# Performance work log

Hardware: AMD Instinct MI355X
Metric: run time of the kernel (lower is better)

Reference implementation:

```python
import jax, jax.numpy as jnp
import numpy as np

B, C, N_OUT = 8, 64, 65536
N_IN = 262144  # unpooled (input) spatial size
K, P = 9, 4    # kernel_size, bilinear interp points


def setup_inputs() -> dict:
    key = jax.random.key(0)
    k1, k2, k3, k4 = jax.random.split(key, 4)
    x = jax.random.normal(k1, (B, C, N_OUT), dtype=jnp.float32)
    idx_mask = jax.random.randint(k2, (B, C, N_OUT), 0, K, dtype=jnp.int32)
    sample_map = jax.random.randint(k3, (N_OUT, K, P), 0, N_IN, dtype=jnp.int32)
    interp_weights = jax.random.uniform(k4, (N_OUT, K, P), dtype=jnp.float32)
    return {"x": x, "idx_mask": idx_mask, "sample_map": sample_map,
            "interp_weights": interp_weights}


def reference(x, idx_mask, sample_map, interp_weights):
    # x: [B,C,N_out] pooled values; idx_mask: [B,C,N_out] winning kernel tap
    # sample_map: [N_out,K,P] int indices into flattened unpooled domain
    # interp_weights: [N_out,K,P] interpolation weights
    b, c, n_out = x.shape
    o_idx = jnp.arange(n_out)[None, None, :]               # [1,1,N_out]
    sel_map = sample_map[o_idx, idx_mask]                  # [B,C,N_out,P]
    sel_w = interp_weights[o_idx, idx_mask]                # [B,C,N_out,P]
    contrib = sel_w * x[..., None]                         # [B,C,N_out,P]
    out = jnp.zeros((b, c, N_IN), dtype=x.dtype)
    bi = jnp.arange(b)[:, None, None, None]
    ci = jnp.arange(c)[None, :, None, None]
    out = out.at[bi, ci, sel_map].add(contrib)             # scatter-add unpool
    return out
```

## Files before the change

kernel.cpp:

```cpp
#include <hip/hip_runtime.h>

#define BB      8
#define CC      64
#define N_OUT   65536
#define N_IN    262144
#define KK      9
#define PP      4
#define NE      (N_OUT * KK * PP)
#define NPLANES 512
#define CHUNK   16
#define NCHUNKS (N_IN / CHUNK)
#define NKEY    NCHUNKS
#define GTH     512
#define NS      (GTH / 32)
#define NFB     128
#define EPB     (NE / NFB)
#define XSTRIDE 800

typedef float f4_t __attribute__((ext_vector_type(4)));

#define WS_OFFSETS 0
#define WS_TOT     16400
#define WS_PRIV    32784
#define WS_HDR     (32784 + NFB * NKEY)
#define WS_ENTR    (2129936 + N_OUT * KK)
#define WS_XK      (((2719760 + 2 * NE) + 31) & ~31)
#define WS_END     (WS_XK + N_OUT * XSTRIDE)

#define XKTILE 16
#define XPAD   520
__global__ __launch_bounds__(256) void k_xk(const float* __restrict__ x,
                                            const int*   __restrict__ idx,
                                            unsigned* __restrict__ xk,
                                            unsigned* __restrict__ hdr) {
    __shared__ float xs[XKTILE * XPAD];
    __shared__ unsigned char ks[XKTILE * XPAD];
    __shared__ unsigned ot[XKTILE * 512];
    __shared__ int cnt[XKTILE][12];
    __shared__ int cur[XKTILE][12];
    __shared__ int cstart[XKTILE][12];
    __shared__ int pstart[XKTILE][12];
    const int t = threadIdx.x;
    const int obase = blockIdx.x * XKTILE;

    for (int i = t; i < XKTILE * 12; i += 256) cnt[i / 12][i % 12] = 0;

    for (int i = t; i < 512 * (XKTILE / 4); i += 256) {
        int p = i >> 2, q = i & 3;
        const size_t g = (size_t)p * N_OUT + obase + 4 * q;
        float4 xv = *(const float4*)(x + g);
        int4   kv = *(const int4*)(idx + g);
        int b = (4 * q) * XPAD + p;
        xs[b] = xv.x; xs[b + XPAD] = xv.y; xs[b + 2 * XPAD] = xv.z; xs[b + 3 * XPAD] = xv.w;
        ks[b] = (unsigned char)kv.x; ks[b + XPAD] = (unsigned char)kv.y;
        ks[b + 2 * XPAD] = (unsigned char)kv.z; ks[b + 3 * XPAD] = (unsigned char)kv.w;
    }
    __syncthreads();
    for (int i = t; i < XKTILE * 512; i += 256) {
        int oo = i >> 9, p = i & 511;
        atomicAdd(&cnt[oo][ks[oo * XPAD + p]], 1);
    }
    __syncthreads();
    if (t < XKTILE) {
        int s = 0, sp = 0;
        for (int k = 0; k < KK; ++k) {
            int c = cnt[t][k];
            cstart[t][k] = s;
            cur[t][k] = s;
            pstart[t][k] = sp;
            hdr[(size_t)(obase + t) * KK + k] = (unsigned)(sp | (c << 16));
            s += c;
            sp += (c + 31) & ~31;
        }
        cstart[t][KK] = 512;
    }
    __syncthreads();
    for (int i = t; i < XKTILE * 512; i += 256) {
        int oo = i >> 9, p = i & 511;
        int k = ks[oo * XPAD + p];
        int pos = atomicAdd(&cur[oo][k], 1);
        unsigned xb = __float_as_uint(xs[oo * XPAD + p]);
        ot[(oo << 9) + pos] = (xb & 0xFFFFFE00u) | (unsigned)p;
    }
    __syncthreads();
    for (int i = t; i < XKTILE * 512; i += 256) {
        int oo = i >> 9, pos = i & 511;
        int k = 0;
        while (k < KK - 1 && pos >= cstart[oo][k + 1]) ++k;
        int dst = pstart[oo][k] + (pos - cstart[oo][k]);
        xk[(size_t)(obase + oo) * XSTRIDE + dst] = ot[(oo << 9) + pos];
    }
}

__global__ __launch_bounds__(1024) void k_histA(const int* __restrict__ smap,
                                                int* __restrict__ priv) {
    __shared__ int h[NKEY];
    const int b = blockIdx.x;
    const int t = threadIdx.x;
    for (int i = t; i < NKEY; i += 1024) h[i] = 0;
    __syncthreads();
    const int e0 = b * EPB;
    #pragma unroll 2
    for (int i = 0; i < EPB / 1024; ++i)
        atomicAdd(&h[smap[e0 + i * 1024 + t] >> 4], 1);
    __syncthreads();
    for (int i = t; i < NKEY; i += 1024) priv[b * NKEY + i] = h[i];
}

__global__ __launch_bounds__(1024) void k_colscan(int* __restrict__ priv,
                                                  int* __restrict__ tot) {
    const int key = blockIdx.x * 1024 + threadIdx.x;
    int run = 0;
    for (int b = 0; b < NFB; ++b) {
        int* p = priv + b * NKEY + key;
        int v = *p; *p = run; run += v;
    }
    tot[key] = run;
}

__global__ __launch_bounds__(1024) void k_scan16k(const int* __restrict__ tot,
                                                  int* __restrict__ offsets) {
    __shared__ int sw[1024];
    const int t = threadIdx.x;
    int4 q0 = ((const int4*)tot)[4 * t + 0];
    int4 q1 = ((const int4*)tot)[4 * t + 1];
    int4 q2 = ((const int4*)tot)[4 * t + 2];
    int4 q3 = ((const int4*)tot)[4 * t + 3];
    int vals[16] = {q0.x, q0.y, q0.z, q0.w, q1.x, q1.y, q1.z, q1.w,
                    q2.x, q2.y, q2.z, q2.w, q3.x, q3.y, q3.z, q3.w};
    int s = 0;
    #pragma unroll
    for (int i = 0; i < 16; ++i) s += vals[i];
    sw[t] = s;
    __syncthreads();
    for (int off = 1; off < 1024; off <<= 1) {
        int v = (t >= off) ? sw[t - off] : 0;
        __syncthreads();
        sw[t] += v;
        __syncthreads();
    }
    int run = sw[t] - s;
    int o[16];
    #pragma unroll
    for (int i = 0; i < 16; ++i) { o[i] = run; run += vals[i]; }
    ((int4*)offsets)[4 * t + 0] = make_int4(o[0], o[1], o[2], o[3]);
    ((int4*)offsets)[4 * t + 1] = make_int4(o[4], o[5], o[6], o[7]);
    ((int4*)offsets)[4 * t + 2] = make_int4(o[8], o[9], o[10], o[11]);
    ((int4*)offsets)[4 * t + 3] = make_int4(o[12], o[13], o[14], o[15]);
    if (t == 1023) offsets[NKEY] = NE;
}

__global__ __launch_bounds__(1024) void k_fillB(const int* __restrict__ smap,
                                                const float* __restrict__ wts,
                                                const int* __restrict__ priv,
                                                const int* __restrict__ offsets,
                                                const unsigned* __restrict__ hdr,
                                                int2* __restrict__ entries) {
    __shared__ int cur[NKEY];
    const int b = blockIdx.x;
    const int t = threadIdx.x;
    for (int i = t; i < NKEY; i += 1024) cur[i] = offsets[i] + priv[b * NKEY + i];
    __syncthreads();
    const int e0 = b * EPB;
    for (int i = 0; i < EPB / 1024; ++i) {
        const int e = e0 + i * 1024 + t;
        const int n = smap[e];
        const int o = e / 36;
        const int r = e - o * 36;
        const int k = r >> 2;
        const unsigned h = hdr[(size_t)o * KK + k];
        const int st = (int)(h & 0xFFFFu);
        const int cn = (int)(h >> 16);
        const unsigned wb = (__float_as_uint(wts[e]) + 0x8000u) >> 16;
        const int pos = atomicAdd(&cur[n >> 4], 1);
        entries[pos] = make_int2((o << 16) | ((n & 15) << 12) | ((cn - 1) << 2),
                                 (int)((wb << 16) | (unsigned)st));
    }
}

#define DECODE(e, o, nl, cn, st, w)                         \
    const int o  = ((unsigned)(e).x) >> 16;                 \
    const int nl = ((e).x >> 12) & 15;                      \
    const int cn = (((e).x >> 2) & 511) + 1;                \
    const int st = (e).y & 0xFFFF;                          \
    const float w = __uint_as_float(((unsigned)(e).y >> 16) << 16);

#define SWZ(p, nl) ((p) ^ ((nl) << 1))
__global__ __launch_bounds__(GTH, 8) void k_gather7(const int* __restrict__ offsets,
                                                    const int2* __restrict__ entries,
                                                    const unsigned* __restrict__ xk,
                                                    float* __restrict__ out) {
    __shared__ float acc[CHUNK * NPLANES];
    const int bid = blockIdx.x;
    const int c = (bid & 7) * (NCHUNKS / 8) + (bid >> 3);
    const int tid = threadIdx.x;
    const int l32 = tid & 31;
    const int sid = tid >> 5;

    f4_t* a4 = (f4_t*)acc;
    for (int i = tid; i < CHUNK * NPLANES / 4; i += GTH) a4[i] = (f4_t){0.f, 0.f, 0.f, 0.f};
    __syncthreads();

    const int j1 = offsets[c + 1];
    int jA = offsets[c] + sid;

    int2 eA = {0, 0}, eB = {0, 0}, eC = {0, 0};
    unsigned xA0 = 0, xA1 = 0, xB0 = 0, xB1 = 0;

    if (jA < j1) eA = entries[jA];
    int jB = jA + NS;
    if (jB < j1) eB = entries[jB];
    if (jA < j1) {
        DECODE(eA, o, nl, cn, st, w)
        const unsigned* r = xk + (size_t)o * XSTRIDE + st;
        if (l32 < cn)      xA0 = r[l32];
        if (l32 + 32 < cn) xA1 = r[l32 + 32];
    }
    if (jB < j1) {
        DECODE(eB, o, nl, cn, st, w)
        const unsigned* r = xk + (size_t)o * XSTRIDE + st;
        if (l32 < cn)      xB0 = r[l32];
        if (l32 + 32 < cn) xB1 = r[l32 + 32];
    }
    int jC = jB + NS;
    if (jC < j1) eC = entries[jC];

    while (jA < j1) {
        unsigned xC0 = 0, xC1 = 0;
        if (jC < j1) {
            DECODE(eC, o, nl, cn, st, w)
            const unsigned* r = xk + (size_t)o * XSTRIDE + st;
            if (l32 < cn)      xC0 = r[l32];
            if (l32 + 32 < cn) xC1 = r[l32 + 32];
        }
        const int jD = jC + NS;
        int2 eD = {0, 0};
        if (jD < j1) eD = entries[jD];

        {
            DECODE(eA, o, nl, cn, st, w)
            if (l32 < cn)
                atomicAdd(&acc[(nl << 9) + SWZ((int)(xA0 & 511), nl)],
                          w * __uint_as_float(xA0 & 0xFFFFFE00u));
            if (l32 + 32 < cn)
                atomicAdd(&acc[(nl << 9) + SWZ((int)(xA1 & 511), nl)],
                          w * __uint_as_float(xA1 & 0xFFFFFE00u));
            if (cn > 64) {
                const unsigned* r = xk + (size_t)o * XSTRIDE + st;
                for (int bb = l32 + 64; bb < cn; bb += 32) {
                    unsigned u = r[bb];
                    atomicAdd(&acc[(nl << 9) + SWZ((int)(u & 511), nl)],
                              w * __uint_as_float(u & 0xFFFFFE00u));
                }
            }
        }
        eA = eB; xA0 = xB0; xA1 = xB1; jA = jB;
        eB = eC; xB0 = xC0; xB1 = xC1; jB = jC;
        eC = eD; jC = jD;
    }
    __syncthreads();

    const int n0 = c << 4;
    for (int i = tid; i < CHUNK * NPLANES / 4; i += GTH) {
        const int p = i >> 2;
        const int nl = (i & 3) << 2;
        float4 v;
        v.x = acc[((nl + 0) << 9) + SWZ(p, nl + 0)];
        v.y = acc[((nl + 1) << 9) + SWZ(p, nl + 1)];
        v.z = acc[((nl + 2) << 9) + SWZ(p, nl + 2)];
        v.w = acc[((nl + 3) << 9) + SWZ(p, nl + 3)];
        *(float4*)(out + (size_t)p * N_IN + n0 + nl) = v;
    }
}

__global__ __launch_bounds__(256) void zero_kernel(float4* __restrict__ out, int n4) {
    int i = blockIdx.x * blockDim.x + threadIdx.x;
    int stride = gridDim.x * blockDim.x;
    const float4 z = {0.f, 0.f, 0.f, 0.f};
    for (; i < n4; i += stride) out[i] = z;
}

__global__ __launch_bounds__(256) void scatter_kernel(
    const float* __restrict__ x, const int* __restrict__ idx_mask,
    const int4* __restrict__ smap, const float4* __restrict__ wts,
    float* __restrict__ out)
{
    const int plane = blockIdx.x >> 8;
    const int o = ((blockIdx.x & 255) << 8) + threadIdx.x;
    const long ibase = (long)plane * N_OUT + o;
    const float xv = x[ibase];
    const int k = idx_mask[ibase];
    const int row = o * KK + k;
    const int4 m = smap[row];
    const float4 w = wts[row];
    float* op = out + (long)plane * N_IN;
    atomicAdd(op + m.x, w.x * xv);
    atomicAdd(op + m.y, w.y * xv);
    atomicAdd(op + m.z, w.z * xv);
    atomicAdd(op + m.w, w.w * xv);
}

extern "C" void kernel_launch(void* const* d_in, const int* in_sizes, int n_in,
                              void* d_out, int out_size, void* d_ws, size_t ws_size,
                              hipStream_t stream) {
    const float* x    = (const float*)d_in[0];
    const int*   idx  = (const int*)d_in[1];
    const int*   smap = (const int*)d_in[2];
    const float* wts  = (const float*)d_in[3];
    float* out = (float*)d_out;

    if (ws_size < (size_t)WS_END * 4) {
        zero_kernel<<<4096, 256, 0, stream>>>((float4*)out, out_size / 4);
        scatter_kernel<<<NPLANES * (N_OUT / 256), 256, 0, stream>>>(
            x, idx, (const int4*)smap, (const float4*)wts, out);
        return;
    }

    int* ws = (int*)d_ws;
    int* offsets   = ws + WS_OFFSETS;
    int* tot       = ws + WS_TOT;
    int* priv      = ws + WS_PRIV;
    unsigned* hdr  = (unsigned*)(ws + WS_HDR);
    int2* entries  = (int2*)(ws + WS_ENTR);
    unsigned* xk   = (unsigned*)(ws + WS_XK);

    k_xk<<<N_OUT / XKTILE, 256, 0, stream>>>(x, idx, xk, hdr);
    k_histA<<<NFB, 1024, 0, stream>>>(smap, priv);
    k_colscan<<<16, 1024, 0, stream>>>(priv, tot);
    k_scan16k<<<1, 1024, 0, stream>>>(tot, offsets);
    k_fillB<<<NFB, 1024, 0, stream>>>(smap, wts, priv, offsets, hdr, entries);

    k_gather7<<<NCHUNKS, GTH, 0, stream>>>(offsets, entries, xk, out);
}
```

Measured before the change: 1.047 ms.

## Pack xk rows densely, use 16-bit packed histogram, double fill blocks

The per-output xk buffer drops its padded per-tap segments (stride 800, each segment rounded to 32) in favour of a dense 512-wide row. The k_xk scatter loop becomes a straight vectorized int4 copy from shared memory, and gather addresses become shifts. The histogram kernel packs two 16-bit counters per shared word, halving its shared memory, and the number of histogram/fill blocks doubles to 256, with extra unrolling. This raises parallelism in the hist and fill phases, at the cost of a larger priv array and a longer column scan, and the gathers lose 32-element alignment.

Measured after the change: 966.0 us. 7.7% less time.

```diff
diff --git a/kernel.cpp b/kernel.cpp
--- a/kernel.cpp
+++ b/kernel.cpp
@@ -13,9 +13,8 @@
 #define NKEY    NCHUNKS
 #define GTH     512
 #define NS      (GTH / 32)
-#define NFB     128
+#define NFB     256
 #define EPB     (NE / NFB)
-#define XSTRIDE 800
 
 typedef float f4_t __attribute__((ext_vector_type(4)));
 
@@ -23,9 +22,9 @@
 #define WS_TOT     16400
 #define WS_PRIV    32784
 #define WS_HDR     (32784 + NFB * NKEY)
-#define WS_ENTR    (2129936 + N_OUT * KK)
-#define WS_XK      (((2719760 + 2 * NE) + 31) & ~31)
-#define WS_END     (WS_XK + N_OUT * XSTRIDE)
+#define WS_ENTR    (4227088 + N_OUT * KK)
+#define WS_XK      (4816912 + 2 * NE)
+#define WS_END     (9535504 + N_OUT * 512)
 
 #define XKTILE 16
 #define XPAD   520
@@ -38,8 +37,6 @@
     __shared__ unsigned ot[XKTILE * 512];
     __shared__ int cnt[XKTILE][12];
     __shared__ int cur[XKTILE][12];
-    __shared__ int cstart[XKTILE][12];
-    __shared__ int pstart[XKTILE][12];
     const int t = threadIdx.x;
     const int obase = blockIdx.x * XKTILE;
 
@@ -62,17 +59,13 @@
     }
     __syncthreads();
     if (t < XKTILE) {
-        int s = 0, sp = 0;
+        int s = 0;
         for (int k = 0; k < KK; ++k) {
             int c = cnt[t][k];
-            cstart[t][k] = s;
             cur[t][k] = s;
-            pstart[t][k] = sp;
-            hdr[(size_t)(obase + t) * KK + k] = (unsigned)(sp | (c << 16));
+            hdr[(size_t)(obase + t) * KK + k] = (unsigned)(s | (c << 16));
             s += c;
-            sp += (c + 31) & ~31;
         }
-        cstart[t][KK] = 512;
     }
     __syncthreads();
     for (int i = t; i < XKTILE * 512; i += 256) {
@@ -83,28 +76,28 @@
         ot[(oo << 9) + pos] = (xb & 0xFFFFFE00u) | (unsigned)p;
     }
     __syncthreads();
-    for (int i = t; i < XKTILE * 512; i += 256) {
-        int oo = i >> 9, pos = i & 511;
-        int k = 0;
-        while (k < KK - 1 && pos >= cstart[oo][k + 1]) ++k;
-        int dst = pstart[oo][k] + (pos - cstart[oo][k]);
-        xk[(size_t)(obase + oo) * XSTRIDE + dst] = ot[(oo << 9) + pos];
+    for (int i = t; i < XKTILE * 128; i += 256) {
+        int oo = i >> 7, c4 = i & 127;
+        ((int4*)(xk + (((size_t)(obase + oo)) << 9)))[c4] = ((const int4*)(ot + (oo << 9)))[c4];
     }
 }
 
 __global__ __launch_bounds__(1024) void k_histA(const int* __restrict__ smap,
                                                 int* __restrict__ priv) {
-    __shared__ int h[NKEY];
+    __shared__ unsigned h32[NKEY / 2];
     const int b = blockIdx.x;
     const int t = threadIdx.x;
-    for (int i = t; i < NKEY; i += 1024) h[i] = 0;
+    for (int i = t; i < NKEY / 2; i += 1024) h32[i] = 0u;
     __syncthreads();
     const int e0 = b * EPB;
-    #pragma unroll 2
-    for (int i = 0; i < EPB / 1024; ++i)
-        atomicAdd(&h[smap[e0 + i * 1024 + t] >> 4], 1);
-    __syncthreads();
-    for (int i = t; i < NKEY; i += 1024) priv[b * NKEY + i] = h[i];
+    #pragma unroll 3
+    for (int i = 0; i < EPB / 1024; ++i) {
+        const int key = smap[e0 + i * 1024 + t] >> 4;
+        atomicAdd(&h32[key >> 1], 1u << ((key & 1) << 4));
+    }
+    __syncthreads();
+    for (int i = t; i < NKEY; i += 1024)
+        priv[b * NKEY + i] = (int)((h32[i >> 1] >> ((i & 1) << 4)) & 0xFFFFu);
 }
 
 __global__ __launch_bounds__(1024) void k_colscan(int* __restrict__ priv,
@@ -162,6 +155,7 @@
     for (int i = t; i < NKEY; i += 1024) cur[i] = offsets[i] + priv[b * NKEY + i];
     __syncthreads();
     const int e0 = b * EPB;
+    #pragma unroll 3
     for (int i = 0; i < EPB / 1024; ++i) {
         const int e = e0 + i * 1024 + t;
         const int n = smap[e];
@@ -212,13 +206,13 @@
     if (jB < j1) eB = entries[jB];
     if (jA < j1) {
         DECODE(eA, o, nl, cn, st, w)
-        const unsigned* r = xk + (size_t)o * XSTRIDE + st;
+        const unsigned* r = xk + ((size_t)o << 9) + st;
         if (l32 < cn)      xA0 = r[l32];
         if (l32 + 32 < cn) xA1 = r[l32 + 32];
     }
     if (jB < j1) {
         DECODE(eB, o, nl, cn, st, w)
-        const unsigned* r = xk + (size_t)o * XSTRIDE + st;
+        const unsigned* r = xk + ((size_t)o << 9) + st;
         if (l32 < cn)      xB0 = r[l32];
         if (l32 + 32 < cn) xB1 = r[l32 + 32];
     }
@@ -229,7 +223,7 @@
         unsigned xC0 = 0, xC1 = 0;
         if (jC < j1) {
             DECODE(eC, o, nl, cn, st, w)
-            const unsigned* r = xk + (size_t)o * XSTRIDE + st;
+            const unsigned* r = xk + ((size_t)o << 9) + st;
             if (l32 < cn)      xC0 = r[l32];
             if (l32 + 32 < cn) xC1 = r[l32 + 32];
         }
@@ -246,7 +240,7 @@
                 atomicAdd(&acc[(nl << 9) + SWZ((int)(xA1 & 511), nl)],
                           w * __uint_as_float(xA1 & 0xFFFFFE00u));
             if (cn > 64) {
-                const unsigned* r = xk + (size_t)o * XSTRIDE + st;
+                const unsigned* r = xk + ((size_t)o << 9) + st;
                 for (int bb = l32 + 64; bb < cn; bb += 32) {
                     unsigned u = r[bb];
                     atomicAdd(&acc[(nl << 9) + SWZ((int)(u & 511), nl)],
```
